# Kernel optimization log

Hardware: AMD Instinct MI355X
Metric: run time of the kernel (lower is better)

Reference implementation:

```python
import jax, jax.numpy as jnp
import numpy as np

B, D, NH, HD, L, P, FF = 2, 256, 8, 32, 4, 4, 1024
SPATIAL = np.array([[100, 100], [50, 50], [25, 25], [13, 13]], dtype=np.int64)
S_TOTAL = int(SPATIAL.prod(1).sum())  # 13294
EPS = 1e-5


def setup_inputs() -> dict:
    key = jax.random.key(0)
    ks = jax.random.split(key, 20)
    std = 0.02
    f32 = jnp.float32
    return {
        "query": jax.random.normal(ks[0], (B, S_TOTAL, D), f32),
        "query_pos": jax.random.normal(ks[1], (B, S_TOTAL, D), f32),
        "valid_ratios": jnp.ones((B, L, 2), f32),
        "spatial_shapes": SPATIAL,
        "level_start_index": np.concatenate([[0], SPATIAL.prod(1).cumsum()[:-1]]).astype(np.int64),
        "W_off": jax.random.normal(ks[2], (D, NH * L * P * 2), f32) * std,
        "b_off": jax.random.normal(ks[3], (NH * L * P * 2,), f32) * std,
        "W_attn": jax.random.normal(ks[4], (D, NH * L * P), f32) * std,
        "b_attn": jax.random.normal(ks[5], (NH * L * P,), f32) * std,
        "W_val": jax.random.normal(ks[6], (D, D), f32) * std,
        "b_val": jnp.zeros((D,), f32),
        "W_out": jax.random.normal(ks[7], (D, D), f32) * std,
        "b_out": jnp.zeros((D,), f32),
        "ln1_g": jnp.ones((D,), f32),
        "ln1_b": jnp.zeros((D,), f32),
        "W1": jax.random.normal(ks[8], (D, FF), f32) * std,
        "b1": jnp.zeros((FF,), f32),
        "W2": jax.random.normal(ks[9], (FF, D), f32) * std,
        "b2": jnp.zeros((D,), f32),
        "ln2_g": jnp.ones((D,), f32),
        "ln2_b": jnp.zeros((D,), f32),
    }


def _layer_norm(x, g, b):
    m = x.mean(-1, keepdims=True)
    v = ((x - m) ** 2).mean(-1, keepdims=True)
    return (x - m) * jax.lax.rsqrt(v + EPS) * g + b


def _bilinear_sample(v, loc, H, W):
    # v: [B, NH, H*W, HD]; loc: [B, NH, S, P, 2] normalized to [0,1]
    # Matches F.grid_sample(bilinear, padding_mode='zeros', align_corners=False)
    x = loc[..., 0] * W - 0.5
    y = loc[..., 1] * H - 0.5
    x0 = jnp.floor(x)
    y0 = jnp.floor(y)
    lx, ly = x - x0, y - y0
    x0i = x0.astype(jnp.int32)
    y0i = y0.astype(jnp.int32)
    x1i, y1i = x0i + 1, y0i + 1

    def corner(yi, xi, w):
        valid = (xi >= 0) & (xi < W) & (yi >= 0) & (yi < H)
        idx = jnp.clip(yi, 0, H - 1) * W + jnp.clip(xi, 0, W - 1)  # [B,NH,S,P]
        b_, h_, s_, p_ = idx.shape
        g = jnp.take_along_axis(v, idx.reshape(b_, h_, s_ * p_)[..., None], axis=2)
        g = g.reshape(b_, h_, s_, p_, -1)
        return g * (w * valid)[..., None]

    return (corner(y0i, x0i, (1 - lx) * (1 - ly)) + corner(y0i, x1i, lx * (1 - ly))
            + corner(y1i, x0i, (1 - lx) * ly) + corner(y1i, x1i, lx * ly))


def _forward(query, query_pos, valid_ratios, spatial_shapes,
             W_off, b_off, W_attn, b_attn, W_val, b_val, W_out, b_out,
             ln1_g, ln1_b, W1, b1, W2, b2, ln2_g, ln2_b):
    ss = np.asarray(spatial_shapes)
    Bq, S, _ = query.shape

    # ----- reference points (per-pixel centers, normalized by valid ratios) -----
    refs = []
    for lvl in range(ss.shape[0]):
        H, W = int(ss[lvl, 0]), int(ss[lvl, 1])
        ry, rx = jnp.meshgrid(jnp.linspace(0.5, H - 0.5, H), jnp.linspace(0.5, W - 0.5, W), indexing='ij')
        vy = valid_ratios[:, lvl, 1][:, None, None]
        vx = valid_ratios[:, lvl, 0][:, None, None]
        ry = ry[None] / (vy * H)
        rx = rx[None] / (vx * W)
        refs.append(jnp.stack((rx, ry), -1).reshape(Bq, H * W, 2))
    ref = jnp.concatenate(refs, 1)  # [B, S, 2] (identical across levels)

    # ----- multi-scale deformable attention -----
    q = query + query_pos
    v = (query @ W_val + b_val).reshape(Bq, S, NH, HD).transpose(0, 2, 1, 3)  # [B,NH,S,HD]
    off = (q @ W_off + b_off).reshape(Bq, S, NH, L, P, 2)
    aw = jax.nn.softmax((q @ W_attn + b_attn).reshape(Bq, S, NH, L * P), -1)
    aw = aw.reshape(Bq, S, NH, L, P)
    normalizer = jnp.asarray(ss[:, ::-1].copy(), jnp.float32)  # (W, H) per level
    loc = ref[:, :, None, None, None, :] + off / normalizer[None, None, None, :, None, :]  # [B,S,NH,L,P,2]

    starts = np.concatenate([[0], ss.prod(1).cumsum()[:-1]])
    out = jnp.zeros((Bq, NH, S, HD), query.dtype)
    for lvl in range(ss.shape[0]):
        H, W = int(ss[lvl, 0]), int(ss[lvl, 1])
        s0 = int(starts[lvl])
        v_l = v[:, :, s0:s0 + H * W]                       # [B,NH,HW,HD]
        loc_l = loc[:, :, :, lvl].transpose(0, 2, 1, 3, 4)  # [B,NH,S,P,2]
        samp = _bilinear_sample(v_l, loc_l, H, W)           # [B,NH,S,P,HD]
        w_l = aw[:, :, :, lvl].transpose(0, 2, 1, 3)        # [B,NH,S,P]
        out = out + (samp * w_l[..., None]).sum(3)
    attn_out = out.transpose(0, 2, 1, 3).reshape(Bq, S, D) @ W_out + b_out

    # ----- residual + LN + FFN + residual + LN -----
    x = _layer_norm(query + attn_out, ln1_g, ln1_b)
    f = jax.nn.relu(x @ W1 + b1) @ W2 + b2
    return _layer_norm(x + f, ln2_g, ln2_b)


def reference(query, query_pos, valid_ratios, spatial_shapes, level_start_index,
              W_off, b_off, W_attn, b_attn, W_val, b_val, W_out, b_out,
              ln1_g, ln1_b, W1, b1, W2, b2, ln2_g, ln2_b):
    return _forward(query, query_pos, valid_ratios, spatial_shapes,
                    W_off, b_off, W_attn, b_attn, W_val, b_val, W_out, b_out,
                    ln1_g, ln1_b, W1, b1, W2, b2, ln2_g, ln2_b)
```

## Files before the change

### kernel.cpp

```cpp
#include <hip/hip_runtime.h>
#include <math.h>

#define R_ROWS 26588
#define S_TOT  13294
#define NHEAD  8
#define NLVL   4
#define EPSF   1e-5f

typedef __attribute__((ext_vector_type(8))) short short8;
typedef __attribute__((ext_vector_type(4))) float f32x4;
typedef __attribute__((ext_vector_type(2))) float f32x2;
typedef unsigned short ushort_t;

__device__ __forceinline__ unsigned short f2bf(float f) {
    unsigned int u = __builtin_bit_cast(unsigned int, f);
    unsigned int r = (u + 0x7FFFu + ((u >> 16) & 1u)) >> 16;
    return (unsigned short)r;
}

__global__ __launch_bounds__(256) void transpose_all_kernel(
    const float* __restrict__ W_val, const float* __restrict__ W_off,
    const float* __restrict__ W_attn, const float* __restrict__ W_out,
    const float* __restrict__ W1, const float* __restrict__ W2,
    ushort_t* __restrict__ wt_val, ushort_t* __restrict__ wt_off,
    ushort_t* __restrict__ wt_attn, ushort_t* __restrict__ wt_out,
    ushort_t* __restrict__ wt_w1, ushort_t* __restrict__ wt_w2)
{
    int bid = blockIdx.x;
    const float* src; ushort_t* dst; int K, N, t;
    if (bid < 64)       { src = W_val;  dst = wt_val;  K = 256;  N = 256;  t = bid; }
    else if (bid < 128) { src = W_off;  dst = wt_off;  K = 256;  N = 256;  t = bid - 64; }
    else if (bid < 160) { src = W_attn; dst = wt_attn; K = 256;  N = 128;  t = bid - 128; }
    else if (bid < 224) { src = W_out;  dst = wt_out;  K = 256;  N = 256;  t = bid - 160; }
    else if (bid < 480) { src = W1;     dst = wt_w1;   K = 256;  N = 1024; t = bid - 224; }
    else                { src = W2;     dst = wt_w2;   K = 1024; N = 256;  t = bid - 480; }
    int nt = N / 32;
    int bn = (t % nt) * 32, bk = (t / nt) * 32;

    __shared__ ushort_t tt[32][33];
    int x = threadIdx.x & 31;
    int y = threadIdx.x >> 5;
#pragma unroll
    for (int i = 0; i < 4; ++i) {
        int k = y + i * 8;
        tt[x][k] = f2bf(src[(long)(bk + k) * N + bn + x]);
    }
    __syncthreads();
#pragma unroll
    for (int i = 0; i < 4; ++i) {
        int n = y + i * 8;
        dst[(long)(bn + n) * K + bk + x] = tt[n][x];
    }
}

__global__ __launch_bounds__(256) void addcvt_kernel(
    const float* __restrict__ q, const float* __restrict__ p,
    ushort_t* __restrict__ qry_bf, ushort_t* __restrict__ qsum_bf, int n4)
{
    int i = blockIdx.x * 256 + threadIdx.x;
    if (i >= n4) return;
    float4 a = ((const float4*)q)[i];
    float4 b = ((const float4*)p)[i];
    uint2 qa, qs;
    qa.x = (unsigned)f2bf(a.x) | ((unsigned)f2bf(a.y) << 16);
    qa.y = (unsigned)f2bf(a.z) | ((unsigned)f2bf(a.w) << 16);
    qs.x = (unsigned)f2bf(a.x + b.x) | ((unsigned)f2bf(a.y + b.y) << 16);
    qs.y = (unsigned)f2bf(a.z + b.z) | ((unsigned)f2bf(a.w + b.w) << 16);
    ((uint2*)qry_bf)[i] = qa;
    ((uint2*)qsum_bf)[i] = qs;
}

#define TBUF 4096

__device__ __forceinline__ void stage_ab(
    const ushort_t* __restrict__ Arow, const ushort_t* __restrict__ Brow,
    int K, int k0, ushort_t* As, ushort_t* Bs, int wave, int lane)
{
    int quadS = lane & 3;
    int rr = lane >> 2;
#pragma unroll
    for (int inst = 0; inst < 2; ++inst) {
        int base_row = wave * 32 + inst * 16;
        int r = base_row + rr;
        int quadG = quadS ^ ((r >> 1) & 3);
        const ushort_t* gp = Arow + (long)r * K + k0 + quadG * 8;
        __builtin_amdgcn_global_load_lds(
            (const __attribute__((address_space(1))) unsigned int*)gp,
            (__attribute__((address_space(3))) unsigned int*)&As[base_row * 32],
            16, 0, 0);
    }
#pragma unroll
    for (int inst = 0; inst < 2; ++inst) {
        int base_row = wave * 32 + inst * 16;
        int r = base_row + rr;
        int quadG = quadS ^ ((r >> 1) & 3);
        const ushort_t* gp = Brow + (long)r * K + k0 + quadG * 8;
        __builtin_amdgcn_global_load_lds(
            (const __attribute__((address_space(1))) unsigned int*)gp,
            (__attribute__((address_space(3))) unsigned int*)&Bs[base_row * 32],
            16, 0, 0);
    }
}

__device__ __forceinline__ void gemm_body(
    ushort_t* As, ushort_t* Bs,
    const ushort_t* __restrict__ A, const ushort_t* __restrict__ Wt,
    const float* __restrict__ bias, void* __restrict__ Cv,
    int M, int N, int K, int bm, int bn, bool out_bf16, bool relu)
{
    const int tid  = threadIdx.x;
    const int wave = tid >> 6;
    const int lane = tid & 63;
    const int l15  = lane & 15;
    const int quad = lane >> 4;
    const int wm   = (wave >> 1) * 64;
    const int wn   = (wave & 1) * 64;

    const ushort_t* Arow = A + (long)bm * K;
    const ushort_t* Brow = Wt + (long)bn * K;

    f32x4 acc[4][4];
#pragma unroll
    for (int i = 0; i < 4; ++i)
#pragma unroll
        for (int j = 0; j < 4; ++j) acc[i][j] = (f32x4)0.0f;

    int aoff[4], boff[4];
#pragma unroll
    for (int mi = 0; mi < 4; ++mi) {
        int r = wm + mi * 16 + l15;
        aoff[mi] = r * 32 + (quad ^ ((r >> 1) & 3)) * 8;
    }
#pragma unroll
    for (int ni = 0; ni < 4; ++ni) {
        int r = wn + ni * 16 + l15;
        boff[ni] = r * 32 + (quad ^ ((r >> 1) & 3)) * 8;
    }

    const int NT = K >> 5;
    stage_ab(Arow, Brow, K, 0, As, Bs, wave, lane);
    int cur = 0;
    for (int t = 0; t < NT; ++t) {
        int nxt = cur + 1; if (nxt == 3) nxt = 0;
        if (t + 1 < NT) {
            stage_ab(Arow, Brow, K, (t + 1) << 5,
                     As + nxt * TBUF, Bs + nxt * TBUF, wave, lane);
            asm volatile("s_waitcnt vmcnt(4)" ::: "memory");
        } else {
            asm volatile("s_waitcnt vmcnt(0)" ::: "memory");
        }
        asm volatile("s_barrier" ::: "memory");

        const ushort_t* Ab = As + cur * TBUF;
        const ushort_t* Bb = Bs + cur * TBUF;
        short8 af[4], bf[4];
#pragma unroll
        for (int mi = 0; mi < 4; ++mi) af[mi] = *(const short8*)&Ab[aoff[mi]];
#pragma unroll
        for (int ni = 0; ni < 4; ++ni) bf[ni] = *(const short8*)&Bb[boff[ni]];
#pragma unroll
        for (int mi = 0; mi < 4; ++mi)
#pragma unroll
            for (int ni = 0; ni < 4; ++ni)
                acc[mi][ni] = __builtin_amdgcn_mfma_f32_16x16x32_bf16(
                    af[mi], bf[ni], acc[mi][ni], 0, 0, 0);
        cur = nxt;
    }

#pragma unroll
    for (int mi = 0; mi < 4; ++mi) {
#pragma unroll
        for (int r = 0; r < 4; ++r) {
            int row = bm + wm + mi * 16 + quad * 4 + r;
            if (row >= M) continue;
#pragma unroll
            for (int ni = 0; ni < 4; ++ni) {
                int col = bn + wn + ni * 16 + l15;
                float vv = acc[mi][ni][r] + bias[col];
                if (relu) vv = fmaxf(vv, 0.f);
                if (out_bf16)
                    ((ushort_t*)Cv)[(long)row * N + col] = f2bf(vv);
                else
                    ((float*)Cv)[(long)row * N + col] = vv;
            }
        }
    }
}

template<bool OUT_BF16, bool RELU>
__global__ __launch_bounds__(256) void gemm_mfma_kernel(
    const ushort_t* __restrict__ A, const ushort_t* __restrict__ Wt,
    const float* __restrict__ bias, void* __restrict__ Cv,
    int M, int N, int K)
{
    __shared__ ushort_t As[3 * TBUF];
    __shared__ ushort_t Bs[3 * TBUF];
    gemm_body(As, Bs, A, Wt, bias, Cv, M, N, K,
              blockIdx.x * 128, blockIdx.y * 128, OUT_BF16, RELU);
}

__global__ __launch_bounds__(256) void proj_kernel(
    const ushort_t* __restrict__ qry_bf, const ushort_t* __restrict__ q_bf,
    const ushort_t* __restrict__ wt_val, const ushort_t* __restrict__ wt_off,
    const ushort_t* __restrict__ wt_attn,
    const float* __restrict__ b_val, const float* __restrict__ b_off,
    const float* __restrict__ b_attn,
    ushort_t* __restrict__ v_bf, float* __restrict__ cb, float* __restrict__ logits)
{
    __shared__ ushort_t As[3 * TBUF];
    __shared__ ushort_t Bs[3 * TBUF];
    int y = blockIdx.y;
    const ushort_t* A; const ushort_t* Wt; const float* bias;
    void* C; bool outbf; int N, bn;
    if (y < 2)      { A = qry_bf; Wt = wt_val;  bias = b_val;  C = v_bf;   outbf = true;  N = 256; bn = y * 128; }
    else if (y < 4) { A = q_bf;   Wt = wt_off;  bias = b_off;  C = cb;     outbf = false; N = 256; bn = (y - 2) * 128; }
    else            { A = q_bf;   Wt = wt_attn; bias = b_attn; C = logits; outbf = false; N = 128; bn = 0; }
    gemm_body(As, Bs, A, Wt, bias, C, R_ROWS, N, 256, blockIdx.x * 128, bn, outbf, false);
}

#define DEF_BLOCKS 3328
#define DEF_CHUNK  416

__global__ __launch_bounds__(256) void deform_sample_kernel(
    const ushort_t* __restrict__ v, const float* __restrict__ off,
    const float* __restrict__ logits, const float* __restrict__ vr,
    ushort_t* __restrict__ out)
{
    const int Hs_[4] = {100, 50, 25, 13};
    const int S0_[4] = {0, 10000, 12500, 13125};

    int wb  = (blockIdx.x & 7) * DEF_CHUNK + (blockIdx.x >> 3);
    int grp = wb * 64 + (threadIdx.x >> 2);
    int j   = threadIdx.x & 3;
    if (grp >= R_ROWS * NHEAD) return;
    int h = grp & 7;
    int r = grp >> 3;
    int b = (r >= S_TOT) ? 1 : 0;
    int s = r - b * S_TOT;

    int lq = (s < 10000) ? 0 : (s < 12500) ? 1 : (s < 13125) ? 2 : 3;
    int t  = s - S0_[lq];
    int Wq = Hs_[lq];
    int iy = t / Wq;
    int jx = t - iy * Wq;
    float vx = vr[(b * NLVL + lq) * 2 + 0];
    float vy = vr[(b * NLVL + lq) * 2 + 1];
    float rx = (jx + 0.5f) / (vx * (float)Wq);
    float ry = (iy + 0.5f) / (vy * (float)Wq);

    const float* offp = off + (long)r * 256 + h * 32;
    float4 oa = ((const float4*)offp)[2 * j];
    float4 ob = ((const float4*)offp)[2 * j + 1];
    float4 lg = ((const float4*)(logits + (long)grp * 16))[j];

    float mx = fmaxf(fmaxf(lg.x, lg.y), fmaxf(lg.z, lg.w));
    mx = fmaxf(mx, __shfl_xor(mx, 1));
    mx = fmaxf(mx, __shfl_xor(mx, 2));
    float e0 = __expf(lg.x - mx), e1 = __expf(lg.y - mx);
    float e2 = __expf(lg.z - mx), e3 = __expf(lg.w - mx);
    float sum = e0 + e1 + e2 + e3;
    sum += __shfl_xor(sum, 1);
    sum += __shfl_xor(sum, 2);
    float inv = 1.f / sum;

    const int   H  = Hs_[j];
    const float fH = (float)H;
    const int   s0 = S0_[j];
    float oxs[4] = {oa.x, oa.z, ob.x, ob.z};
    float oys[4] = {oa.y, oa.w, ob.y, ob.w};
    float wts[4] = {e0 * inv, e1 * inv, e2 * inv, e3 * inv};
    float pw0[4], pw1[4], pw2[4], pw3[4];
    int   pi0[4], pi1[4], pi2[4], pi3[4];
#pragma unroll
    for (int i = 0; i < 4; ++i) {
        float x = rx * fH + oxs[i] - 0.5f;
        float y = ry * fH + oys[i] - 0.5f;
        float xf = floorf(x), yf = floorf(y);
        float lx = x - xf, ly = y - yf;
        int x0 = (int)xf, y0 = (int)yf;
        bool xv0 = (x0 >= 0) & (x0 < H);
        bool xv1 = (x0 >= -1) & (x0 < H - 1);
        bool yv0 = (y0 >= 0) & (y0 < H);
        bool yv1 = (y0 >= -1) & (y0 < H - 1);
        float w = wts[i];
        pw0[i] = (xv0 & yv0) ? (1.f - lx) * (1.f - ly) * w : 0.f;
        pw1[i] = (xv1 & yv0) ? lx * (1.f - ly) * w : 0.f;
        pw2[i] = (xv0 & yv1) ? (1.f - lx) * ly * w : 0.f;
        pw3[i] = (xv1 & yv1) ? lx * ly * w : 0.f;
        int xc0 = min(max(x0, 0), H - 1), xc1 = min(max(x0 + 1, 0), H - 1);
        int yc0 = min(max(y0, 0), H - 1), yc1 = min(max(y0 + 1, 0), H - 1);
        pi0[i] = s0 + yc0 * H + xc0;
        pi1[i] = s0 + yc0 * H + xc1;
        pi2[i] = s0 + yc1 * H + xc0;
        pi3[i] = s0 + yc1 * H + xc1;
    }

    const ushort_t* vb = v + ((long)b * S_TOT) * 256 + h * 32 + j * 8;
    f32x2 acc2[4];
#pragma unroll
    for (int c = 0; c < 4; ++c) acc2[c] = (f32x2)0.0f;

#define ACC_CORNER(IDX, WGT) do {                                            \
        uint4 g = *(const uint4*)&vb[(long)(IDX) * 256];                     \
        unsigned uu0 = g.x, uu1 = g.y, uu2 = g.z, uu3 = g.w;                 \
        f32x2 gv;                                                            \
        gv.x = __builtin_bit_cast(float, uu0 << 16);                         \
        gv.y = __builtin_bit_cast(float, uu0 & 0xFFFF0000u);                 \
        acc2[0] += gv * (WGT);                                               \
        gv.x = __builtin_bit_cast(float, uu1 << 16);                         \
        gv.y = __builtin_bit_cast(float, uu1 & 0xFFFF0000u);                 \
        acc2[1] += gv * (WGT);                                               \
        gv.x = __builtin_bit_cast(float, uu2 << 16);                         \
        gv.y = __builtin_bit_cast(float, uu2 & 0xFFFF0000u);                 \
        acc2[2] += gv * (WGT);                                               \
        gv.x = __builtin_bit_cast(float, uu3 << 16);                         \
        gv.y = __builtin_bit_cast(float, uu3 & 0xFFFF0000u);                 \
        acc2[3] += gv * (WGT);                                               \
    } while (0)

#pragma unroll
    for (int i = 0; i < 4; ++i) {
#pragma unroll
        for (int j2 = 0; j2 < 4; ++j2) {
            float w00 = __shfl(pw0[i], j2, 4);
            float w01 = __shfl(pw1[i], j2, 4);
            float w10 = __shfl(pw2[i], j2, 4);
            float w11 = __shfl(pw3[i], j2, 4);
            int   i00 = __shfl(pi0[i], j2, 4);
            int   i01 = __shfl(pi1[i], j2, 4);
            int   i10 = __shfl(pi2[i], j2, 4);
            int   i11 = __shfl(pi3[i], j2, 4);
            ACC_CORNER(i00, w00);
            ACC_CORNER(i01, w01);
            ACC_CORNER(i10, w10);
            ACC_CORNER(i11, w11);
        }
    }
#undef ACC_CORNER

    uint4 o;
    o.x = (unsigned)f2bf(acc2[0].x) | ((unsigned)f2bf(acc2[0].y) << 16);
    o.y = (unsigned)f2bf(acc2[1].x) | ((unsigned)f2bf(acc2[1].y) << 16);
    o.z = (unsigned)f2bf(acc2[2].x) | ((unsigned)f2bf(acc2[2].y) << 16);
    o.w = (unsigned)f2bf(acc2[3].x) | ((unsigned)f2bf(acc2[3].y) << 16);
    *(uint4*)&out[(long)r * 256 + h * 32 + j * 8] = o;
}

template<bool DUAL>
__global__ __launch_bounds__(256) void add_ln_kernel(
    const float* __restrict__ a, const float* __restrict__ b,
    const float* __restrict__ g, const float* __restrict__ beta,
    float* __restrict__ outf, ushort_t* __restrict__ outb)
{
    int row = blockIdx.x;
    int tid = threadIdx.x;
    float x = a[(long)row * 256 + tid] + b[(long)row * 256 + tid];
    float s1 = x, s2 = x * x;
#pragma unroll
    for (int o = 32; o > 0; o >>= 1) {
        s1 += __shfl_down(s1, o, 64);
        s2 += __shfl_down(s2, o, 64);
    }
    __shared__ float sh1[4], sh2[4];
    int w = tid >> 6;
    if ((tid & 63) == 0) { sh1[w] = s1; sh2[w] = s2; }
    __syncthreads();
    float t1 = sh1[0] + sh1[1] + sh1[2] + sh1[3];
    float t2 = sh2[0] + sh2[1] + sh2[2] + sh2[3];
    float mean = t1 * (1.f / 256.f);
    float var  = t2 * (1.f / 256.f) - mean * mean;
    float inv  = rsqrtf(var + EPSF);
    float y = (x - mean) * inv * g[tid] + beta[tid];
    outf[(long)row * 256 + tid] = y;
    if (DUAL) outb[(long)row * 256 + tid] = f2bf(y);
}

extern "C" void kernel_launch(void* const* d_in, const int* in_sizes, int n_in,
                              void* d_out, int out_size, void* d_ws, size_t ws_size,
                              hipStream_t stream)
{
    const float* query  = (const float*)d_in[0];
    const float* qpos   = (const float*)d_in[1];
    const float* vr     = (const float*)d_in[2];
    const float* W_off  = (const float*)d_in[5];
    const float* b_off  = (const float*)d_in[6];
    const float* W_attn = (const float*)d_in[7];
    const float* b_attn = (const float*)d_in[8];
    const float* W_val  = (const float*)d_in[9];
    const float* b_val  = (const float*)d_in[10];
    const float* W_out  = (const float*)d_in[11];
    const float* b_out  = (const float*)d_in[12];
    const float* ln1g   = (const float*)d_in[13];
    const float* ln1b   = (const float*)d_in[14];
    const float* W1     = (const float*)d_in[15];
    const float* b1     = (const float*)d_in[16];
    const float* W2     = (const float*)d_in[17];
    const float* b2     = (const float*)d_in[18];
    const float* ln2g   = (const float*)d_in[19];
    const float* ln2b   = (const float*)d_in[20];
    float* out = (float*)d_out;

    float* ws = (float*)d_ws;
    const long R128 = (long)R_ROWS * 128;
    ushort_t* q_bf    = (ushort_t*)(ws);
    ushort_t* qry_bf  = (ushort_t*)(ws + R128);
    ushort_t* v_bf    = (ushort_t*)(ws + 2 * R128);
    float*    logits  = ws + 3 * R128;
    ushort_t* h_bf    = (ushort_t*)(ws);
    float*    cb      = ws + 4 * R128;
    ushort_t* samp_bf = (ushort_t*)(ws + 6 * R128);
    float*    xb      = ws + 7 * R128;
    ushort_t* wt      = (ushort_t*)(ws + 9 * R128);
    ushort_t* wt_val  = wt;
    ushort_t* wt_off  = wt + 65536;
    ushort_t* wt_attn = wt + 131072;
    ushort_t* wt_out  = wt + 163840;
    ushort_t* wt_w1   = wt + 229376;
    ushort_t* wt_w2   = wt + 491520;

    dim3 blk(256);
    const int MB = (R_ROWS + 127) / 128;

    transpose_all_kernel<<<736, blk, 0, stream>>>(
        W_val, W_off, W_attn, W_out, W1, W2,
        wt_val, wt_off, wt_attn, wt_out, wt_w1, wt_w2);
    addcvt_kernel<<<(R_ROWS * 64 + 255) / 256, blk, 0, stream>>>(
        query, qpos, qry_bf, q_bf, R_ROWS * 64);
    proj_kernel<<<dim3(MB, 5), blk, 0, stream>>>(
        qry_bf, q_bf, wt_val, wt_off, wt_attn, b_val, b_off, b_attn,
        v_bf, cb, logits);
    deform_sample_kernel<<<DEF_BLOCKS, blk, 0, stream>>>(
        v_bf, cb, logits, vr, samp_bf);
    gemm_mfma_kernel<false, false><<<dim3(MB, 2), blk, 0, stream>>>(
        samp_bf, wt_out, b_out, cb, R_ROWS, 256, 256);
    add_ln_kernel<true><<<R_ROWS, blk, 0, stream>>>(query, cb, ln1g, ln1b, xb, samp_bf);
    gemm_mfma_kernel<true, true><<<dim3(MB, 8), blk, 0, stream>>>(
        samp_bf, wt_w1, b1, h_bf, R_ROWS, 1024, 256);
    gemm_mfma_kernel<false, false><<<dim3(MB, 2), blk, 0, stream>>>(
        h_bf, wt_w2, b2, cb, R_ROWS, 256, 1024);
    add_ln_kernel<false><<<R_ROWS, blk, 0, stream>>>(xb, cb, ln2g, ln2b, out, nullptr);
}
```

Before: 326.9 us.

## Use 64-row GEMM tiles for N=256, LDS corner tables in sampler, wave-per-row LayerNorm

The GEMM is templated on M-tile size, and the two N=256 GEMMs (out-proj, W2) now use 64-row tiles, doubling block count to fill more CUs. The deformable sampler now stores per-point corner weights and indices in shared memory instead of 128 lane shuffles, with a barrier. Out-of-range threads are clamped instead of returning early so the barrier is safe. LayerNorm now handles one row per wave with float4 loads and xor-shuffle reductions, which removes the block barrier and shared memory.

```diff
diff --git a/kernel.cpp b/kernel.cpp
--- a/kernel.cpp
+++ b/kernel.cpp
@@ -70,17 +70,17 @@
     ((uint2*)qsum_bf)[i] = qs;
 }
 
-#define TBUF 4096
-
+template<int MT>
 __device__ __forceinline__ void stage_ab(
     const ushort_t* __restrict__ Arow, const ushort_t* __restrict__ Brow,
     int K, int k0, ushort_t* As, ushort_t* Bs, int wave, int lane)
 {
     int quadS = lane & 3;
     int rr = lane >> 2;
-#pragma unroll
-    for (int inst = 0; inst < 2; ++inst) {
-        int base_row = wave * 32 + inst * 16;
+    constexpr int AI = MT / 64;
+#pragma unroll
+    for (int inst = 0; inst < AI; ++inst) {
+        int base_row = wave * (MT / 4) + inst * 16;
         int r = base_row + rr;
         int quadG = quadS ^ ((r >> 1) & 3);
         const ushort_t* gp = Arow + (long)r * K + k0 + quadG * 8;
@@ -102,32 +102,36 @@
     }
 }
 
+template<int MT>
 __device__ __forceinline__ void gemm_body(
     ushort_t* As, ushort_t* Bs,
     const ushort_t* __restrict__ A, const ushort_t* __restrict__ Wt,
     const float* __restrict__ bias, void* __restrict__ Cv,
     int M, int N, int K, int bm, int bn, bool out_bf16, bool relu)
 {
+    constexpr int TBA = MT * 32;
+    constexpr int TBB = 4096;
+    constexpr int MFR = MT / 32;
     const int tid  = threadIdx.x;
     const int wave = tid >> 6;
     const int lane = tid & 63;
     const int l15  = lane & 15;
     const int quad = lane >> 4;
-    const int wm   = (wave >> 1) * 64;
+    const int wm   = (wave >> 1) * (MT / 2);
     const int wn   = (wave & 1) * 64;
 
     const ushort_t* Arow = A + (long)bm * K;
     const ushort_t* Brow = Wt + (long)bn * K;
 
-    f32x4 acc[4][4];
-#pragma unroll
-    for (int i = 0; i < 4; ++i)
+    f32x4 acc[MFR][4];
+#pragma unroll
+    for (int i = 0; i < MFR; ++i)
 #pragma unroll
         for (int j = 0; j < 4; ++j) acc[i][j] = (f32x4)0.0f;
 
-    int aoff[4], boff[4];
-#pragma unroll
-    for (int mi = 0; mi < 4; ++mi) {
+    int aoff[MFR], boff[4];
+#pragma unroll
+    for (int mi = 0; mi < MFR; ++mi) {
         int r = wm + mi * 16 + l15;
         aoff[mi] = r * 32 + (quad ^ ((r >> 1) & 3)) * 8;
     }
@@ -138,28 +142,31 @@
     }
 
     const int NT = K >> 5;
-    stage_ab(Arow, Brow, K, 0, As, Bs, wave, lane);
+    stage_ab<MT>(Arow, Brow, K, 0, As, Bs, wave, lane);
     int cur = 0;
     for (int t = 0; t < NT; ++t) {
         int nxt = cur + 1; if (nxt == 3) nxt = 0;
         if (t + 1 < NT) {
-            stage_ab(Arow, Brow, K, (t + 1) << 5,
-                     As + nxt * TBUF, Bs + nxt * TBUF, wave, lane);
-            asm volatile("s_waitcnt vmcnt(4)" ::: "memory");
+            stage_ab<MT>(Arow, Brow, K, (t + 1) << 5,
+                         As + nxt * TBA, Bs + nxt * TBB, wave, lane);
+            if constexpr (MT == 128)
+                asm volatile("s_waitcnt vmcnt(4)" ::: "memory");
+            else
+                asm volatile("s_waitcnt vmcnt(3)" ::: "memory");
         } else {
             asm volatile("s_waitcnt vmcnt(0)" ::: "memory");
         }
         asm volatile("s_barrier" ::: "memory");
 
-        const ushort_t* Ab = As + cur * TBUF;
-        const ushort_t* Bb = Bs + cur * TBUF;
-        short8 af[4], bf[4];
-#pragma unroll
-        for (int mi = 0; mi < 4; ++mi) af[mi] = *(const short8*)&Ab[aoff[mi]];
+        const ushort_t* Ab = As + cur * TBA;
+        const ushort_t* Bb = Bs + cur * TBB;
+        short8 af[MFR], bf[4];
+#pragma unroll
+        for (int mi = 0; mi < MFR; ++mi) af[mi] = *(const short8*)&Ab[aoff[mi]];
 #pragma unroll
         for (int ni = 0; ni < 4; ++ni) bf[ni] = *(const short8*)&Bb[boff[ni]];
 #pragma unroll
-        for (int mi = 0; mi < 4; ++mi)
+        for (int mi = 0; mi < MFR; ++mi)
 #pragma unroll
             for (int ni = 0; ni < 4; ++ni)
                 acc[mi][ni] = __builtin_amdgcn_mfma_f32_16x16x32_bf16(
@@ -168,7 +175,7 @@
     }
 
 #pragma unroll
-    for (int mi = 0; mi < 4; ++mi) {
+    for (int mi = 0; mi < MFR; ++mi) {
 #pragma unroll
         for (int r = 0; r < 4; ++r) {
             int row = bm + wm + mi * 16 + quad * 4 + r;
@@ -187,16 +194,16 @@
     }
 }
 
-template<bool OUT_BF16, bool RELU>
+template<int MT, bool OUT_BF16, bool RELU>
 __global__ __launch_bounds__(256) void gemm_mfma_kernel(
     const ushort_t* __restrict__ A, const ushort_t* __restrict__ Wt,
     const float* __restrict__ bias, void* __restrict__ Cv,
     int M, int N, int K)
 {
-    __shared__ ushort_t As[3 * TBUF];
-    __shared__ ushort_t Bs[3 * TBUF];
-    gemm_body(As, Bs, A, Wt, bias, Cv, M, N, K,
-              blockIdx.x * 128, blockIdx.y * 128, OUT_BF16, RELU);
+    __shared__ ushort_t As[3 * MT * 32];
+    __shared__ ushort_t Bs[3 * 4096];
+    gemm_body<MT>(As, Bs, A, Wt, bias, Cv, M, N, K,
+                  blockIdx.x * MT, blockIdx.y * 128, OUT_BF16, RELU);
 }
 
 __global__ __launch_bounds__(256) void proj_kernel(
@@ -207,15 +214,15 @@
     const float* __restrict__ b_attn,
     ushort_t* __restrict__ v_bf, float* __restrict__ cb, float* __restrict__ logits)
 {
-    __shared__ ushort_t As[3 * TBUF];
-    __shared__ ushort_t Bs[3 * TBUF];
+    __shared__ ushort_t As[3 * 4096];
+    __shared__ ushort_t Bs[3 * 4096];
     int y = blockIdx.y;
     const ushort_t* A; const ushort_t* Wt; const float* bias;
     void* C; bool outbf; int N, bn;
     if (y < 2)      { A = qry_bf; Wt = wt_val;  bias = b_val;  C = v_bf;   outbf = true;  N = 256; bn = y * 128; }
     else if (y < 4) { A = q_bf;   Wt = wt_off;  bias = b_off;  C = cb;     outbf = false; N = 256; bn = (y - 2) * 128; }
     else            { A = q_bf;   Wt = wt_attn; bias = b_attn; C = logits; outbf = false; N = 128; bn = 0; }
-    gemm_body(As, Bs, A, Wt, bias, C, R_ROWS, N, 256, blockIdx.x * 128, bn, outbf, false);
+    gemm_body<128>(As, Bs, A, Wt, bias, C, R_ROWS, N, 256, blockIdx.x * 128, bn, outbf, false);
 }
 
 #define DEF_BLOCKS 3328
@@ -226,13 +233,18 @@
     const float* __restrict__ logits, const float* __restrict__ vr,
     ushort_t* __restrict__ out)
 {
+    __shared__ float4 gw[64][17];
+    __shared__ int4   gi[64][17];
+
     const int Hs_[4] = {100, 50, 25, 13};
     const int S0_[4] = {0, 10000, 12500, 13125};
 
     int wb  = (blockIdx.x & 7) * DEF_CHUNK + (blockIdx.x >> 3);
-    int grp = wb * 64 + (threadIdx.x >> 2);
+    int g   = threadIdx.x >> 2;
     int j   = threadIdx.x & 3;
-    if (grp >= R_ROWS * NHEAD) return;
+    int grp = wb * 64 + g;
+    const int total = R_ROWS * NHEAD;
+    if (grp >= total) grp = total - 1;
     int h = grp & 7;
     int r = grp >> 3;
     int b = (r >= S_TOT) ? 1 : 0;
@@ -269,8 +281,6 @@
     float oxs[4] = {oa.x, oa.z, ob.x, ob.z};
     float oys[4] = {oa.y, oa.w, ob.y, ob.w};
     float wts[4] = {e0 * inv, e1 * inv, e2 * inv, e3 * inv};
-    float pw0[4], pw1[4], pw2[4], pw3[4];
-    int   pi0[4], pi1[4], pi2[4], pi3[4];
 #pragma unroll
     for (int i = 0; i < 4; ++i) {
         float x = rx * fH + oxs[i] - 0.5f;
@@ -283,17 +293,22 @@
         bool yv0 = (y0 >= 0) & (y0 < H);
         bool yv1 = (y0 >= -1) & (y0 < H - 1);
         float w = wts[i];
-        pw0[i] = (xv0 & yv0) ? (1.f - lx) * (1.f - ly) * w : 0.f;
-        pw1[i] = (xv1 & yv0) ? lx * (1.f - ly) * w : 0.f;
-        pw2[i] = (xv0 & yv1) ? (1.f - lx) * ly * w : 0.f;
-        pw3[i] = (xv1 & yv1) ? lx * ly * w : 0.f;
+        float4 wv;
+        wv.x = (xv0 & yv0) ? (1.f - lx) * (1.f - ly) * w : 0.f;
+        wv.y = (xv1 & yv0) ? lx * (1.f - ly) * w : 0.f;
+        wv.z = (xv0 & yv1) ? (1.f - lx) * ly * w : 0.f;
+        wv.w = (xv1 & yv1) ? lx * ly * w : 0.f;
         int xc0 = min(max(x0, 0), H - 1), xc1 = min(max(x0 + 1, 0), H - 1);
         int yc0 = min(max(y0, 0), H - 1), yc1 = min(max(y0 + 1, 0), H - 1);
-        pi0[i] = s0 + yc0 * H + xc0;
-        pi1[i] = s0 + yc0 * H + xc1;
-        pi2[i] = s0 + yc1 * H + xc0;
-        pi3[i] = s0 + yc1 * H + xc1;
-    }
+        int4 iv;
+        iv.x = s0 + yc0 * H + xc0;
+        iv.y = s0 + yc0 * H + xc1;
+        iv.z = s0 + yc1 * H + xc0;
+        iv.w = s0 + yc1 * H + xc1;
+        gw[g][j * 4 + i] = wv;
+        gi[g][j * 4 + i] = iv;
+    }
+    __syncthreads();
 
     const ushort_t* vb = v + ((long)b * S_TOT) * 256 + h * 32 + j * 8;
     f32x2 acc2[4];
@@ -301,8 +316,8 @@
     for (int c = 0; c < 4; ++c) acc2[c] = (f32x2)0.0f;
 
 #define ACC_CORNER(IDX, WGT) do {                                            \
-        uint4 g = *(const uint4*)&vb[(long)(IDX) * 256];                     \
-        unsigned uu0 = g.x, uu1 = g.y, uu2 = g.z, uu3 = g.w;                 \
+        uint4 gld = *(const uint4*)&vb[(long)(IDX) * 256];                   \
+        unsigned uu0 = gld.x, uu1 = gld.y, uu2 = gld.z, uu3 = gld.w;         \
         f32x2 gv;                                                            \
         gv.x = __builtin_bit_cast(float, uu0 << 16);                         \
         gv.y = __builtin_bit_cast(float, uu0 & 0xFFFF0000u);                 \
@@ -318,23 +333,14 @@
         acc2[3] += gv * (WGT);                                               \
     } while (0)
 
-#pragma unroll
-    for (int i = 0; i < 4; ++i) {
-#pragma unroll
-        for (int j2 = 0; j2 < 4; ++j2) {
-            float w00 = __shfl(pw0[i], j2, 4);
-            float w01 = __shfl(pw1[i], j2, 4);
-            float w10 = __shfl(pw2[i], j2, 4);
-            float w11 = __shfl(pw3[i], j2, 4);
-            int   i00 = __shfl(pi0[i], j2, 4);
-            int   i01 = __shfl(pi1[i], j2, 4);
-            int   i10 = __shfl(pi2[i], j2, 4);
-            int   i11 = __shfl(pi3[i], j2, 4);
-            ACC_CORNER(i00, w00);
-            ACC_CORNER(i01, w01);
-            ACC_CORNER(i10, w10);
-            ACC_CORNER(i11, w11);
-        }
+#pragma unroll 4
+    for (int p = 0; p < 16; ++p) {
+        float4 w = gw[g][p];
+        int4   ix = gi[g][p];
+        ACC_CORNER(ix.x, w.x);
+        ACC_CORNER(ix.y, w.y);
+        ACC_CORNER(ix.z, w.z);
+        ACC_CORNER(ix.w, w.w);
     }
 #undef ACC_CORNER
 
@@ -352,27 +358,37 @@
     const float* __restrict__ g, const float* __restrict__ beta,
     float* __restrict__ outf, ushort_t* __restrict__ outb)
 {
-    int row = blockIdx.x;
-    int tid = threadIdx.x;
-    float x = a[(long)row * 256 + tid] + b[(long)row * 256 + tid];
-    float s1 = x, s2 = x * x;
-#pragma unroll
-    for (int o = 32; o > 0; o >>= 1) {
-        s1 += __shfl_down(s1, o, 64);
-        s2 += __shfl_down(s2, o, 64);
-    }
-    __shared__ float sh1[4], sh2[4];
-    int w = tid >> 6;
-    if ((tid & 63) == 0) { sh1[w] = s1; sh2[w] = s2; }
-    __syncthreads();
-    float t1 = sh1[0] + sh1[1] + sh1[2] + sh1[3];
-    float t2 = sh2[0] + sh2[1] + sh2[2] + sh2[3];
-    float mean = t1 * (1.f / 256.f);
-    float var  = t2 * (1.f / 256.f) - mean * mean;
+    int row  = blockIdx.x * 4 + (threadIdx.x >> 6);
+    int lane = threadIdx.x & 63;
+    long base = (long)row * 256 + lane * 4;
+    float4 av = *(const float4*)&a[base];
+    float4 bv = *(const float4*)&b[base];
+    float4 x;
+    x.x = av.x + bv.x; x.y = av.y + bv.y; x.z = av.z + bv.z; x.w = av.w + bv.w;
+    float s1 = x.x + x.y + x.z + x.w;
+    float s2 = x.x * x.x + x.y * x.y + x.z * x.z + x.w * x.w;
+#pragma unroll
+    for (int o = 1; o < 64; o <<= 1) {
+        s1 += __shfl_xor(s1, o);
+        s2 += __shfl_xor(s2, o);
+    }
+    float mean = s1 * (1.f / 256.f);
+    float var  = s2 * (1.f / 256.f) - mean * mean;
     float inv  = rsqrtf(var + EPSF);
-    float y = (x - mean) * inv * g[tid] + beta[tid];
-    outf[(long)row * 256 + tid] = y;
-    if (DUAL) outb[(long)row * 256 + tid] = f2bf(y);
+    float4 gv = *(const float4*)&g[lane * 4];
+    float4 be = *(const float4*)&beta[lane * 4];
+    float4 y;
+    y.x = (x.x - mean) * inv * gv.x + be.x;
+    y.y = (x.y - mean) * inv * gv.y + be.y;
+    y.z = (x.z - mean) * inv * gv.z + be.z;
+    y.w = (x.w - mean) * inv * gv.w + be.w;
+    *(float4*)&outf[base] = y;
+    if (DUAL) {
+        uint2 o;
+        o.x = (unsigned)f2bf(y.x) | ((unsigned)f2bf(y.y) << 16);
+        o.y = (unsigned)f2bf(y.z) | ((unsigned)f2bf(y.w) << 16);
+        *(uint2*)&outb[base] = o;
+    }
 }
 
 extern "C" void kernel_launch(void* const* d_in, const int* in_sizes, int n_in,
@@ -419,24 +435,27 @@
     ushort_t* wt_w2   = wt + 491520;
 
     dim3 blk(256);
-    const int MB = (R_ROWS + 127) / 128;
+    const int MB128 = (R_ROWS + 127) / 128;
+    const int MB64  = (R_ROWS + 63) / 64;
 
     transpose_all_kernel<<<736, blk, 0, stream>>>(
         W_val, W_off, W_attn, W_out, W1, W2,
         wt_val, wt_off, wt_attn, wt_out, wt_w1, wt_w2);
     addcvt_kernel<<<(R_ROWS * 64 + 255) / 256, blk, 0, stream>>>(
         query, qpos, qry_bf, q_bf, R_ROWS * 64);
-    proj_kernel<<<dim3(MB, 5), blk, 0, stream>>>(
+    proj_kernel<<<dim3(MB128, 5), blk, 0, stream>>>(
         qry_bf, q_bf, wt_val, wt_off, wt_attn, b_val, b_off, b_attn,
         v_bf, cb, logits);
     deform_sample_kernel<<<DEF_BLOCKS, blk, 0, stream>>>(
         v_bf, cb, logits, vr, samp_bf);
-    gemm_mfma_kernel<false, false><<<dim3(MB, 2), blk, 0, stream>>>(
+    gemm_mfma_kernel<64, false, false><<<dim3(MB64, 2), blk, 0, stream>>>(
         samp_bf, wt_out, b_out, cb, R_ROWS, 256, 256);
-    add_ln_kernel<true><<<R_ROWS, blk, 0, stream>>>(query, cb, ln1g, ln1b, xb, samp_bf);
-    gemm_mfma_kernel<true, true><<<dim3(MB, 8), blk, 0, stream>>>(
+    add_ln_kernel<true><<<R_ROWS / 4, blk, 0, stream>>>(
+        query, cb, ln1g, ln1b, xb, samp_bf);
+    gemm_mfma_kernel<128, true, true><<<dim3(MB128, 8), blk, 0, stream>>>(
         samp_bf, wt_w1, b1, h_bf, R_ROWS, 1024, 256);
-    gemm_mfma_kernel<false, false><<<dim3(MB, 2), blk, 0, stream>>>(
+    gemm_mfma_kernel<64, false, false><<<dim3(MB64, 2), blk, 0, stream>>>(
         h_bf, wt_w2, b2, cb, R_ROWS, 256, 1024);
-    add_ln_kernel<false><<<R_ROWS, blk, 0, stream>>>(xb, cb, ln2g, ln2b, out, nullptr);
-}
+    add_ln_kernel<false><<<R_ROWS / 4, blk, 0, stream>>>(
+        xb, cb, ln2g, ln2b, out, nullptr);
+}
```

New measurement: 330.0 us. About the same (+1.0%).
